# Optimization experiments

Hardware: AMD Instinct MI355X
Metric: run time of the kernel (lower is better)

## Reference

```python
import jax, jax.numpy as jnp
import numpy as np

B, S, VOCAB, HID, NH, L, SPAN = 4, 512, 25, 512, 8, 12, 512
HEAD = HID // NH
FF = 4 * HID
EPS = 1e-7  # DebertaV2 layer_norm_eps


def _ln(x, g, b):
    m = x.mean(-1, keepdims=True)
    v = ((x - m) ** 2).mean(-1, keepdims=True)
    return (x - m) / jnp.sqrt(v + EPS) * g + b


def setup_inputs() -> dict:
    key = jax.random.key(0)
    ks = iter(jax.random.split(key, 16))
    w = lambda shape: jax.random.normal(next(ks), shape, jnp.float32) * 0.05
    return {
        "x": jax.random.randint(next(ks), (B, S), 0, VOCAB),
        "attention_mask": jnp.ones((B, S), jnp.int32),
        "word_emb": w((VOCAB, HID)),
        "emb_ln_g": jnp.ones((HID,), jnp.float32),
        "emb_ln_b": jnp.zeros((HID,), jnp.float32),
        "rel_emb": w((2 * SPAN, HID)),
        "Wq": w((L, HID, HID)), "bq": jnp.zeros((L, HID), jnp.float32),
        "Wk": w((L, HID, HID)), "bk": jnp.zeros((L, HID), jnp.float32),
        "Wv": w((L, HID, HID)), "bv": jnp.zeros((L, HID), jnp.float32),
        "Wpk": w((L, HID, HID)), "bpk": jnp.zeros((L, HID), jnp.float32),
        "Wpq": w((L, HID, HID)), "bpq": jnp.zeros((L, HID), jnp.float32),
        "Wo": w((L, HID, HID)), "bo": jnp.zeros((L, HID), jnp.float32),
        "ln1_g": jnp.ones((L, HID), jnp.float32), "ln1_b": jnp.zeros((L, HID), jnp.float32),
        "W1": w((L, HID, FF)), "b1": jnp.zeros((L, FF), jnp.float32),
        "W2": w((L, FF, HID)), "b2": jnp.zeros((L, HID), jnp.float32),
        "ln2_g": jnp.ones((L, HID), jnp.float32), "ln2_b": jnp.zeros((L, HID), jnp.float32),
        "cls_w": w((VOCAB, HID)), "cls_b": jnp.zeros((VOCAB,), jnp.float32),
    }


def _forward(x, attention_mask, word_emb, emb_ln_g, emb_ln_b, rel_emb,
             Wq, bq, Wk, bk, Wv, bv, Wpk, bpk, Wpq, bpq, Wo, bo,
             ln1_g, ln1_b, W1, b1, W2, b2, ln2_g, ln2_b, cls_w, cls_b):
    mask = attention_mask.astype(jnp.float32)
    # embeddings: word only (position_biased_input=False), LN, then masked
    h = _ln(word_emb[x], emb_ln_g, emb_ln_b) * mask[..., None]

    rel = jnp.arange(S)[:, None] - jnp.arange(S)[None, :]          # q_pos - k_pos
    c2p_idx = jnp.clip(rel + SPAN, 0, 2 * SPAN - 1)[None, None]    # [1,1,S,S]
    p2c_idx = jnp.clip(-rel + SPAN, 0, 2 * SPAN - 1)[None, None]
    attm = (mask[:, None, None, :] * mask[:, None, :, None]) > 0   # [B,1,S,S]
    scale = jnp.sqrt(jnp.float32(HEAD * 3))                        # scale_factor = 1 + len(pos_att_type)
    neg = jnp.finfo(jnp.float32).min

    def heads(t):  # [B,S,HID] -> [B,NH,S,HEAD]
        return t.reshape(B, S, NH, HEAD).transpose(0, 2, 1, 3)

    for l in range(L):
        q = heads(h @ Wq[l] + bq[l])
        k = heads(h @ Wk[l] + bk[l])
        v = heads(h @ Wv[l] + bv[l])
        # projected relative-position embeddings: [NH, 2*SPAN, HEAD]
        pk = (rel_emb @ Wpk[l] + bpk[l]).reshape(2 * SPAN, NH, HEAD).transpose(1, 0, 2)
        pq = (rel_emb @ Wpq[l] + bpq[l]).reshape(2 * SPAN, NH, HEAD).transpose(1, 0, 2)

        scores = jnp.einsum('bhqd,bhkd->bhqk', q, k)
        # c2p: query content vs key position, gathered at clamp(rel+span)
        c2p = jnp.take_along_axis(jnp.einsum('bhqd,hpd->bhqp', q, pk), c2p_idx, axis=-1)
        # p2c: key content vs query position, gathered at clamp(-rel+span) then transposed
        p2c = jnp.take_along_axis(jnp.einsum('bhkd,hpd->bhkp', k, pq), p2c_idx, axis=-1)
        scores = (scores + c2p + jnp.swapaxes(p2c, -1, -2)) / scale

        scores = jnp.where(attm, scores, neg)
        probs = jnp.where(attm, jax.nn.softmax(scores, axis=-1), 0.0)  # XSoftmax
        ctx = jnp.einsum('bhqk,bhkd->bhqd', probs, v).transpose(0, 2, 1, 3).reshape(B, S, HID)
        h = _ln(ctx @ Wo[l] + bo[l] + h, ln1_g[l], ln1_b[l])
        f = jax.nn.gelu(h @ W1[l] + b1[l], approximate=False) @ W2[l] + b2[l]
        h = _ln(f + h, ln2_g[l], ln2_b[l])

    logits = h @ cls_w.T + cls_b
    return h, logits


def reference(x, attention_mask, word_emb, emb_ln_g, emb_ln_b, rel_emb,
              Wq, bq, Wk, bk, Wv, bv, Wpk, bpk, Wpq, bpq, Wo, bo,
              ln1_g, ln1_b, W1, b1, W2, b2, ln2_g, ln2_b, cls_w, cls_b):
    return _forward(x, attention_mask, word_emb, emb_ln_g, emb_ln_b, rel_emb,
                    Wq, bq, Wk, bk, Wv, bv, Wpk, bpk, Wpq, bpq, Wo, bo,
                    ln1_g, ln1_b, W1, b1, W2, b2, ln2_g, ln2_b, cls_w, cls_b)
```

## Files before the change

kernel.cpp:

```cpp
#include <hip/hip_runtime.h>
#include <hip/hip_bf16.h>

#define BATCH  4
#define SEQ    512
#define TOK    (BATCH*SEQ)
#define HID    512
#define NHEAD  8
#define HEAD   64
#define FFDIM  2048
#define NLAYER 12
#define SPAN2  1024
#define VOCAB  25
#define LNEPS  1e-7f
#define NEG_BIG -3.0e38f

typedef __attribute__((ext_vector_type(8))) short bf16x8;
typedef __attribute__((ext_vector_type(4))) float floatx4;

#define MFMA16(a, b, c) __builtin_amdgcn_mfma_f32_16x16x32_bf16((a), (b), (c), 0, 0, 0)

__device__ __forceinline__ float b2f(unsigned short u) {
    return __uint_as_float(((unsigned int)u) << 16);
}
__device__ __forceinline__ unsigned short f2b(float f) {
    __hip_bfloat16 h = __float2bfloat16(f);
    return *(unsigned short*)&h;
}

__device__ __forceinline__ float wave_sum(float v) {
    #pragma unroll
    for (int o = 1; o < 64; o <<= 1) v += __shfl_xor(v, o);
    return v;
}

__device__ __forceinline__ void ln_finish(const float (&v)[8], const float* __restrict__ g,
                                          const float* __restrict__ bb, int lane, float maskf,
                                          size_t base, float* __restrict__ h,
                                          unsigned short* __restrict__ hb) {
    float sum = 0.f;
    #pragma unroll
    for (int j = 0; j < 8; j++) sum += v[j];
    float mean = wave_sum(sum) * (1.0f / HID);
    float d[8]; float var = 0.f;
    #pragma unroll
    for (int j = 0; j < 8; j++) { d[j] = v[j] - mean; var += d[j] * d[j]; }
    float rstd = rsqrtf(wave_sum(var) * (1.0f / HID) + LNEPS);
    const float* gp = g + lane * 8; const float* bp = bb + lane * 8;
    float4 g0 = *(const float4*)gp, g1 = *(const float4*)(gp + 4);
    float4 b0 = *(const float4*)bp, b1 = *(const float4*)(bp + 4);
    float gg[8] = {g0.x, g0.y, g0.z, g0.w, g1.x, g1.y, g1.z, g1.w};
    float bv[8] = {b0.x, b0.y, b0.z, b0.w, b1.x, b1.y, b1.z, b1.w};
    float o8[8];
    #pragma unroll
    for (int j = 0; j < 8; j++) o8[j] = (d[j] * rstd * gg[j] + bv[j]) * maskf;
    *(float4*)(h + base)     = make_float4(o8[0], o8[1], o8[2], o8[3]);
    *(float4*)(h + base + 4) = make_float4(o8[4], o8[5], o8[6], o8[7]);
    uint4 pb;
    pb.x = (unsigned int)f2b(o8[0]) | ((unsigned int)f2b(o8[1]) << 16);
    pb.y = (unsigned int)f2b(o8[2]) | ((unsigned int)f2b(o8[3]) << 16);
    pb.z = (unsigned int)f2b(o8[4]) | ((unsigned int)f2b(o8[5]) << 16);
    pb.w = (unsigned int)f2b(o8[6]) | ((unsigned int)f2b(o8[7]) << 16);
    *(uint4*)(hb + base) = pb;
}

__global__ void embed_ln_kernel(const int* __restrict__ x, const int* __restrict__ am,
                                const float* __restrict__ word_emb,
                                const float* __restrict__ g, const float* __restrict__ bb,
                                float* __restrict__ h, unsigned short* __restrict__ hb) {
    int wv = threadIdx.x >> 6, lane = threadIdx.x & 63;
    int t = blockIdx.x * 4 + wv;
    const float* we = word_emb + (size_t)x[t] * HID + lane * 8;
    float4 va = *(const float4*)we, vb2 = *(const float4*)(we + 4);
    float v[8] = {va.x, va.y, va.z, va.w, vb2.x, vb2.y, vb2.z, vb2.w};
    ln_finish(v, g, bb, lane, (float)am[t], (size_t)t * HID + lane * 8, h, hb);
}

__global__ void add_ln_kernel(const float* __restrict__ tmp,
                              const float* __restrict__ g, const float* __restrict__ bb,
                              float* __restrict__ h, unsigned short* __restrict__ hb) {
    int wv = threadIdx.x >> 6, lane = threadIdx.x & 63;
    int t = blockIdx.x * 4 + wv;
    size_t base = (size_t)t * HID + lane * 8;
    float4 ta = *(const float4*)(tmp + base), tb = *(const float4*)(tmp + base + 4);
    float4 ha = *(const float4*)(h + base),  hbb = *(const float4*)(h + base + 4);
    float v[8] = {ta.x + ha.x, ta.y + ha.y, ta.z + ha.z, ta.w + ha.w,
                  tb.x + hbb.x, tb.y + hbb.y, tb.z + hbb.z, tb.w + hbb.w};
    ln_finish(v, g, bb, lane, 1.0f, base, h, hb);
}

__global__ void add_ln2_kernel(const float* __restrict__ t1a, const float* __restrict__ t1b,
                               const float* __restrict__ g, const float* __restrict__ bb,
                               float* __restrict__ h, unsigned short* __restrict__ hb) {
    int wv = threadIdx.x >> 6, lane = threadIdx.x & 63;
    int t = blockIdx.x * 4 + wv;
    size_t base = (size_t)t * HID + lane * 8;
    float4 aa = *(const float4*)(t1a + base), ab = *(const float4*)(t1a + base + 4);
    float4 ba = *(const float4*)(t1b + base), bbv = *(const float4*)(t1b + base + 4);
    float4 ha = *(const float4*)(h + base),  hb2 = *(const float4*)(h + base + 4);
    float v[8] = {aa.x + ba.x + ha.x, aa.y + ba.y + ha.y, aa.z + ba.z + ha.z, aa.w + ba.w + ha.w,
                  ab.x + bbv.x + hb2.x, ab.y + bbv.y + hb2.y, ab.z + bbv.z + hb2.z, ab.w + bbv.w + hb2.w};
    ln_finish(v, g, bb, lane, 1.0f, base, h, hb);
}

__global__ void cvt_rel_kernel(const float* __restrict__ in, unsigned short* __restrict__ out) {
    int i = (blockIdx.x * 256 + threadIdx.x) * 4;
    float4 v = *(const float4*)(in + i);
    out[i] = f2b(v.x); out[i+1] = f2b(v.y); out[i+2] = f2b(v.z); out[i+3] = f2b(v.w);
}

__global__ void tcvt_kernel(const float* __restrict__ in, unsigned short* __restrict__ out,
                            int K, int N) {
    __shared__ float tile[32][33];
    int l = blockIdx.z;
    const float* ip = in + (size_t)l * K * N;
    unsigned short* op = out + (size_t)l * K * N;
    int kb = blockIdx.y * 32, nb = blockIdx.x * 32;
    int tx = threadIdx.x, ty = threadIdx.y;
    #pragma unroll
    for (int i = 0; i < 32; i += 8) tile[ty + i][tx] = ip[(size_t)(kb + ty + i) * N + nb + tx];
    __syncthreads();
    #pragma unroll
    for (int i = 0; i < 32; i += 8) op[(size_t)(nb + ty + i) * K + kb + tx] = f2b(tile[tx][ty + i]);
}

__global__ void tcvt6_kernel(const float* __restrict__ Wq, const float* __restrict__ Wk,
                             const float* __restrict__ Wv, const float* __restrict__ Wpk,
                             const float* __restrict__ Wpq, const float* __restrict__ Wo,
                             unsigned short* __restrict__ out) {
    __shared__ float tile[32][33];
    int z = blockIdx.z, l = z / 6, w = z - l * 6;
    const float* src = w == 0 ? Wq : w == 1 ? Wk : w == 2 ? Wv : w == 3 ? Wpk : w == 4 ? Wpq : Wo;
    const float* ip = src + (size_t)l * HID * HID;
    unsigned short* op = out + ((size_t)w * NLAYER + l) * HID * HID;
    int kb = blockIdx.y * 32, nb = blockIdx.x * 32;
    int tx = threadIdx.x, ty = threadIdx.y;
    #pragma unroll
    for (int i = 0; i < 32; i += 8) tile[ty + i][tx] = ip[(size_t)(kb + ty + i) * HID + nb + tx];
    __syncthreads();
    #pragma unroll
    for (int i = 0; i < 32; i += 8) op[(size_t)(nb + ty + i) * HID + kb + tx] = f2b(tile[tx][ty + i]);
}

__device__ __forceinline__ void gemm_core128(
    const unsigned short* __restrict__ A, const unsigned short* __restrict__ Bt,
    int row0, int col0, int K, int kbeg, int kend,
    floatx4 (&acc)[4][2], unsigned short (&As)[2][128][72], unsigned short (&Bs)[2][64][72]) {
    int tid = threadIdx.x;
    int lane = tid & 63, wid = tid >> 6;
    int wm = wid >> 1, wn = wid & 1;
    int m16 = lane & 15, quad = lane >> 4;
    int asr = tid >> 1, asc = (tid & 1) * 32;
    int bsr = tid >> 2, bsc = (tid & 3) * 16;
    const unsigned short* Ag = A + (size_t)(row0 + asr) * K + asc;
    const unsigned short* Bg = Bt + (size_t)(col0 + bsr) * K + bsc;

    uint4 a0 = *(const uint4*)(Ag + kbeg),      a1 = *(const uint4*)(Ag + kbeg + 8);
    uint4 a2 = *(const uint4*)(Ag + kbeg + 16), a3 = *(const uint4*)(Ag + kbeg + 24);
    uint4 b0 = *(const uint4*)(Bg + kbeg),      b1 = *(const uint4*)(Bg + kbeg + 8);
    *(uint4*)&As[0][asr][asc]      = a0;
    *(uint4*)&As[0][asr][asc + 8]  = a1;
    *(uint4*)&As[0][asr][asc + 16] = a2;
    *(uint4*)&As[0][asr][asc + 24] = a3;
    *(uint4*)&Bs[0][bsr][bsc]      = b0;
    *(uint4*)&Bs[0][bsr][bsc + 8]  = b1;
    __syncthreads();

    int cur = 0;
    for (int k0 = kbeg; k0 < kend; k0 += 64) {
        int k1 = k0 + 64;
        bool more = k1 < kend;
        if (more) {
            a0 = *(const uint4*)(Ag + k1);      a1 = *(const uint4*)(Ag + k1 + 8);
            a2 = *(const uint4*)(Ag + k1 + 16); a3 = *(const uint4*)(Ag + k1 + 24);
            b0 = *(const uint4*)(Bg + k1);      b1 = *(const uint4*)(Bg + k1 + 8);
        }
        #pragma unroll
        for (int kk = 0; kk < 2; kk++) {
            bf16x8 bf0 = *(const bf16x8*)&Bs[cur][wn * 32 + m16][kk * 32 + quad * 8];
            bf16x8 bf1 = *(const bf16x8*)&Bs[cur][wn * 32 + 16 + m16][kk * 32 + quad * 8];
            #pragma unroll
            for (int mi = 0; mi < 4; mi++) {
                bf16x8 af = *(const bf16x8*)&As[cur][wm * 64 + mi * 16 + m16][kk * 32 + quad * 8];
                acc[mi][0] = MFMA16(af, bf0, acc[mi][0]);
                acc[mi][1] = MFMA16(af, bf1, acc[mi][1]);
            }
        }
        if (more) {
            *(uint4*)&As[cur ^ 1][asr][asc]      = a0;
            *(uint4*)&As[cur ^ 1][asr][asc + 8]  = a1;
            *(uint4*)&As[cur ^ 1][asr][asc + 16] = a2;
            *(uint4*)&As[cur ^ 1][asr][asc + 24] = a3;
            *(uint4*)&Bs[cur ^ 1][bsr][bsc]      = b0;
            *(uint4*)&Bs[cur ^ 1][bsr][bsc + 8]  = b1;
            __syncthreads();
            cur ^= 1;
        }
    }
}

template<bool OUT_BF16, bool GELU, int SPLITK>
__global__ __launch_bounds__(256, 2) void gemm_bt2(
    const unsigned short* __restrict__ A, const unsigned short* __restrict__ Bt,
    const float* __restrict__ bias, void* __restrict__ Cp, int N, int K) {
    __shared__ unsigned short As[2][128][72], Bs[2][64][72];
    int row0 = blockIdx.y * 128, col0 = blockIdx.x * 64;
    int kseg = K / SPLITK;
    int kbeg = kseg * blockIdx.z, kend = kbeg + kseg;
    floatx4 acc[4][2];
    #pragma unroll
    for (int mi = 0; mi < 4; mi++)
        #pragma unroll
        for (int ni = 0; ni < 2; ni++) acc[mi][ni] = (floatx4){0.f, 0.f, 0.f, 0.f};
    gemm_core128(A, Bt, row0, col0, K, kbeg, kend, acc, As, Bs);

    int tid = threadIdx.x, lane = tid & 63, wid = tid >> 6;
    int wm = wid >> 1, wn = wid & 1, m16 = lane & 15, quad = lane >> 4;
    size_t outoff = (size_t)blockIdx.z * (size_t)(gridDim.y << 7) * N;
    #pragma unroll
    for (int ni = 0; ni < 2; ni++) {
        int colg = col0 + wn * 32 + ni * 16 + m16;
        float bval = (SPLITK == 1 || blockIdx.z == 0) ? bias[colg] : 0.0f;
        #pragma unroll
        for (int mi = 0; mi < 4; mi++) {
            #pragma unroll
            for (int r = 0; r < 4; r++) {
                int rowg = row0 + wm * 64 + mi * 16 + quad * 4 + r;
                float v = acc[mi][ni][r] + bval;
                if (GELU) v = 0.5f * v * (1.0f + erff(v * 0.70710678118654752f));
                if (OUT_BF16) ((unsigned short*)Cp)[(size_t)rowg * N + colg] = f2b(v);
                else          ((float*)Cp)[outoff + (size_t)rowg * N + colg] = v;
            }
        }
    }
}

__global__ __launch_bounds__(256, 2) void qkvp_gemm(
    const unsigned short* __restrict__ hb, const unsigned short* __restrict__ relb,
    const unsigned short* __restrict__ Wqt, const unsigned short* __restrict__ Wkt,
    const unsigned short* __restrict__ Wvt, const unsigned short* __restrict__ Wpkt,
    const unsigned short* __restrict__ Wpqt,
    const float* __restrict__ bq, const float* __restrict__ bk, const float* __restrict__ bv,
    const float* __restrict__ bpk, const float* __restrict__ bpq,
    unsigned short* __restrict__ qb, unsigned short* __restrict__ kb,
    unsigned short* __restrict__ vb, unsigned short* __restrict__ pkb,
    unsigned short* __restrict__ pqb) {
    __shared__ unsigned short As[2][128][72], Bs[2][64][72];
    int bid = blockIdx.x;
    int xcd = bid & 7, slot = bid >> 3;
    int op, j;
    if (xcd < 6) { op = xcd >> 1; j = slot * 2 + (xcd & 1); }
    else         { op = xcd - 3;  j = slot; }
    int trow = j >> 3, tcol = j & 7;
    const unsigned short* A; const unsigned short* Bt; const float* bias; unsigned short* C;
    if (op < 3) {
        A = hb;
        Bt   = op == 0 ? Wqt : op == 1 ? Wkt : Wvt;
        bias = op == 0 ? bq  : op == 1 ? bk  : bv;
        C    = op == 0 ? qb  : op == 1 ? kb  : vb;
    } else {
        A = relb;
        Bt   = op == 3 ? Wpkt : Wpqt;
        bias = op == 3 ? bpk  : bpq;
        C    = op == 3 ? pkb  : pqb;
    }
    floatx4 acc[4][2];
    #pragma unroll
    for (int mi = 0; mi < 4; mi++)
        #pragma unroll
        for (int ni = 0; ni < 2; ni++) acc[mi][ni] = (floatx4){0.f, 0.f, 0.f, 0.f};
    gemm_core128(A, Bt, trow * 128, tcol * 64, HID, 0, HID, acc, As, Bs);

    int tid = threadIdx.x, lane = tid & 63, wid = tid >> 6;
    int wm = wid >> 1, wn = wid & 1, m16 = lane & 15, quad = lane >> 4;
    #pragma unroll
    for (int ni = 0; ni < 2; ni++) {
        int colg = tcol * 64 + wn * 32 + ni * 16 + m16;
        float bval = bias[colg];
        #pragma unroll
        for (int mi = 0; mi < 4; mi++) {
            #pragma unroll
            for (int r = 0; r < 4; r++) {
                int rowg = trow * 128 + wm * 64 + mi * 16 + quad * 4 + r;
                C[(size_t)rowg * HID + colg] = f2b(acc[mi][ni][r] + bval);
            }
        }
    }
}

template<bool OUT_BF16, bool GELU>
__global__ __launch_bounds__(256) void mfma_gemm(
    const unsigned short* __restrict__ A, const float* __restrict__ B,
    const float* __restrict__ bias, void* __restrict__ Cp, int N, int K) {
    __shared__ unsigned short As[64][72];
    __shared__ unsigned short Bs[64][72];
    int tid = threadIdx.x;
    int lane = tid & 63, wid = tid >> 6;
    int wm = wid >> 1, wn = wid & 1;
    int row0 = blockIdx.y * 64, col0 = blockIdx.x * 64;
    int m16 = lane & 15, quad = lane >> 4;

    int ar = tid >> 2, ac = (tid & 3) << 4;
    int bk = (tid >> 3) << 1, bn = (tid & 7) << 3;

    const unsigned short* Ag = A + (size_t)(row0 + ar) * K + ac;
    const float* Bg = B + (size_t)bk * N + col0 + bn;

    floatx4 acc[2][2];
    #pragma unroll
    for (int mi = 0; mi < 2; mi++)
        #pragma unroll
        for (int ni = 0; ni < 2; ni++) acc[mi][ni] = (floatx4){0.f, 0.f, 0.f, 0.f};

    for (int k0 = 0; k0 < K; k0 += 64) {
        uint4 av0 = *(const uint4*)(Ag + k0);
        uint4 av1 = *(const uint4*)(Ag + k0 + 8);
        const float* br0 = Bg + (size_t)k0 * N;
        const float* br1 = br0 + N;
        float4 b00 = *(const float4*)br0, b01 = *(const float4*)(br0 + 4);
        float4 b10 = *(const float4*)br1, b11 = *(const float4*)(br1 + 4);
        *(uint4*)&As[ar][ac] = av0;
        *(uint4*)&As[ar][ac + 8] = av1;
        float lo[8] = {b00.x, b00.y, b00.z, b00.w, b01.x, b01.y, b01.z, b01.w};
        float hi[8] = {b10.x, b10.y, b10.z, b10.w, b11.x, b11.y, b11.z, b11.w};
        #pragma unroll
        for (int i = 0; i < 8; i++) {
            unsigned int p = (unsigned int)f2b(lo[i]) | ((unsigned int)f2b(hi[i]) << 16);
            *(unsigned int*)&Bs[bn + i][bk] = p;
        }
        __syncthreads();
        #pragma unroll
        for (int kk = 0; kk < 2; kk++) {
            bf16x8 a0 = *(const bf16x8*)&As[wm * 32 + m16][kk * 32 + quad * 8];
            bf16x8 a1 = *(const bf16x8*)&As[wm * 32 + 16 + m16][kk * 32 + quad * 8];
            bf16x8 b0 = *(const bf16x8*)&Bs[wn * 32 + m16][kk * 32 + quad * 8];
            bf16x8 b1 = *(const bf16x8*)&Bs[wn * 32 + 16 + m16][kk * 32 + quad * 8];
            acc[0][0] = MFMA16(a0, b0, acc[0][0]);
            acc[0][1] = MFMA16(a0, b1, acc[0][1]);
            acc[1][0] = MFMA16(a1, b0, acc[1][0]);
            acc[1][1] = MFMA16(a1, b1, acc[1][1]);
        }
        __syncthreads();
    }
    #pragma unroll
    for (int ni = 0; ni < 2; ni++) {
        int colg = col0 + wn * 32 + ni * 16 + m16;
        float bv = bias[colg];
        #pragma unroll
        for (int mi = 0; mi < 2; mi++) {
            #pragma unroll
            for (int r = 0; r < 4; r++) {
                int rowg = row0 + wm * 32 + mi * 16 + quad * 4 + r;
                float v = acc[mi][ni][r] + bv;
                if (GELU) v = 0.5f * v * (1.0f + erff(v * 0.70710678118654752f));
                if (OUT_BF16) ((unsigned short*)Cp)[(size_t)rowg * N + colg] = f2b(v);
                else          ((float*)Cp)[(size_t)rowg * N + colg] = v;
            }
        }
    }
}

__global__ __launch_bounds__(256, 2) void attn_kernel(
    const unsigned short* __restrict__ Q, const unsigned short* __restrict__ K,
    const unsigned short* __restrict__ V,
    const unsigned short* __restrict__ PK, const unsigned short* __restrict__ PQ,
    const int* __restrict__ am, unsigned short* __restrict__ ctx) {
    __shared__ unsigned short Ks[2][32][72];
    __shared__ unsigned short Vt[2][64][40];
    __shared__ float Afs[4][16][49];
    __shared__ float Bfs[4][32][50];
    __shared__ unsigned short Pls[4][16][40];
    __shared__ int mkk[2][32];
    __shared__ float mergeML[2][2][16];

    int bid = blockIdx.x;
    int hh = bid & 7;
    int b  = (bid >> 3) & 3;
    int q0 = (bid >> 5) * 32;
    int tid = threadIdx.x;
    int lane = tid & 63, wave = tid >> 6;
    int u = wave >> 1;
    int s = wave & 1;
    int quad = lane >> 4, m16 = lane & 15;
    const float inv_scale = 0.07216878364870323f;

    const unsigned short* qg = Q + (size_t)(b * SEQ + q0 + u * 16 + m16) * HID + hh * HEAD;
    bf16x8 qf0 = *(const bf16x8*)(qg + quad * 8);
    bf16x8 qf1 = *(const bf16x8*)(qg + 32 + quad * 8);

    int sr = tid >> 3;
    int sc = (tid & 7) * 8;
    int vkey = ((sc >> 3) & 3) << 3;

    floatx4 accO[4];
    #pragma unroll
    for (int nt = 0; nt < 4; nt++) accO[nt] = (floatx4){0.f, 0.f, 0.f, 0.f};
    float mreg[4] = {NEG_BIG, NEG_BIG, NEG_BIG, NEG_BIG};
    float lreg[4] = {0.f, 0.f, 0.f, 0.f};

    auto loadPQ = [&](int t, bf16x8 (&pkf)[3][2], bf16x8 (&pqf)[3][2]) {
        int P0  = q0 - 32 * t + 481;
        int P20 = 32 * t - q0 + 481;
        int Jb  = 16 - 16 * u;
        #pragma unroll
        for (int nt = 0; nt < 3; nt++) {
            int prow = P0 + 16 * u + nt * 16 + m16;
            const unsigned short* pg = PK + (size_t)prow * HID + hh * HEAD + quad * 8;
            pkf[nt][0] = *(const bf16x8*)pg;
            pkf[nt][1] = *(const bf16x8*)(pg + 32);
            int prow2 = P20 + Jb + nt * 16 + m16;
            if (prow2 > 1023) prow2 = 1023;
            const unsigned short* pg2 = PQ + (size_t)prow2 * HID + hh * HEAD + quad * 8;
            pqf[nt][0] = *(const bf16x8*)pg2;
            pqf[nt][1] = *(const bf16x8*)(pg2 + 32);
        }
    };

    auto stageKV = [&](int ph) {
        #pragma unroll
        for (int sl = 0; sl < 2; sl++) {
            int k0 = ph * 64 + sl * 32;
            const unsigned short* kg = K + (size_t)(b * SEQ + k0 + sr) * HID + hh * HEAD + sc;
            *(uint4*)&Ks[sl][sr][sc] = *(const uint4*)kg;
            uint4 vv = *(const uint4*)(V + (size_t)(b * SEQ + k0 + sr) * HID + hh * HEAD + sc);
            unsigned short* vp = (unsigned short*)&vv;
            #pragma unroll
            for (int j = 0; j < 8; j++) Vt[sl][sc + j][sr ^ vkey] = vp[j];
        }
        if (tid < 64) mkk[tid >> 5][tid & 31] = am[b * SEQ + ph * 64 + tid];
    };

    auto computePhase = [&](bf16x8 (&pkf)[3][2], bf16x8 (&pqf)[3][2]) {
        floatx4 accS[2];
        accS[0] = (floatx4){0.f, 0.f, 0.f, 0.f};
        accS[1] = (floatx4){0.f, 0.f, 0.f, 0.f};
        #pragma unroll
        for (int n = 0; n < 2; n++) {
            bf16x8 kfa = *(const bf16x8*)&Ks[s][n * 16 + m16][quad * 8];
            bf16x8 kfb = *(const bf16x8*)&Ks[s][n * 16 + m16][32 + quad * 8];
            accS[n] = MFMA16(qf0, kfa, accS[n]);
            accS[n] = MFMA16(qf1, kfb, accS[n]);
        }
        {
            floatx4 accA[3];
            #pragma unroll
            for (int nt = 0; nt < 3; nt++) {
                accA[nt] = (floatx4){0.f, 0.f, 0.f, 0.f};
                accA[nt] = MFMA16(qf0, pkf[nt][0], accA[nt]);
                accA[nt] = MFMA16(qf1, pkf[nt][1], accA[nt]);
            }
            #pragma unroll
            for (int nt = 0; nt < 3; nt++)
                #pragma unroll
                for (int r = 0; r < 4; r++)
                    Afs[wave][quad * 4 + r][nt * 16 + m16] = accA[nt][r];
        }
        {
            floatx4 accB[2][3];
            #pragma unroll
            for (int mt = 0; mt < 2; mt++) {
                bf16x8 afa = *(const bf16x8*)&Ks[s][mt * 16 + m16][quad * 8];
                bf16x8 afb = *(const bf16x8*)&Ks[s][mt * 16 + m16][32 + quad * 8];
                #pragma unroll
                for (int nt = 0; nt < 3; nt++) {
                    accB[mt][nt] = (floatx4){0.f, 0.f, 0.f, 0.f};
                    accB[mt][nt] = MFMA16(afa, pqf[nt][0], accB[mt][nt]);
                    accB[mt][nt] = MFMA16(afb, pqf[nt][1], accB[mt][nt]);
                }
            }
            #pragma unroll
            for (int mt = 0; mt < 2; mt++)
                #pragma unroll
                for (int nt = 0; nt < 3; nt++)
                    #pragma unroll
                    for (int r = 0; r < 4; r++)
                        Bfs[wave][mt * 16 + quad * 4 + r][nt * 16 + m16] = accB[mt][nt][r];
        }
        float sv[2][4];
        float tmax[4] = {NEG_BIG, NEG_BIG, NEG_BIG, NEG_BIG};
        #pragma unroll
        for (int n = 0; n < 2; n++) {
            #pragma unroll
            for (int r = 0; r < 4; r++) {
                int qq = quad * 4 + r;
                int kc = n * 16 + m16;
                float av = Afs[wave][qq][qq - kc + 31];
                float bv = Bfs[wave][kc][kc - qq + 15];
                float x = (accS[n][r] + av + bv) * inv_scale;
                x = mkk[s][kc] ? x : NEG_BIG;
                sv[n][r] = x;
                tmax[r] = fmaxf(tmax[r], x);
            }
        }
        float alpha[4], psum[4];
        #pragma unroll
        for (int r = 0; r < 4; r++) {
            float tm = tmax[r];
            tm = fmaxf(tm, __shfl_xor(tm, 1));
            tm = fmaxf(tm, __shfl_xor(tm, 2));
            tm = fmaxf(tm, __shfl_xor(tm, 4));
            tm = fmaxf(tm, __shfl_xor(tm, 8));
            float mo = mreg[r];
            float mn = fmaxf(mo, tm);
            alpha[r] = __expf(mo - mn);
            mreg[r] = mn;
        }
        #pragma unroll
        for (int r = 0; r < 4; r++) psum[r] = 0.f;
        #pragma unroll
        for (int n = 0; n < 2; n++) {
            #pragma unroll
            for (int r = 0; r < 4; r++) {
                float p = (sv[n][r] > -1.5e38f) ? __expf(sv[n][r] - mreg[r]) : 0.0f;
                unsigned short pb = f2b(p);
                Pls[wave][quad * 4 + r][n * 16 + m16] = pb;
                psum[r] += b2f(pb);
            }
        }
        #pragma unroll
        for (int r = 0; r < 4; r++) {
            float ps = psum[r];
            ps += __shfl_xor(ps, 1);
            ps += __shfl_xor(ps, 2);
            ps += __shfl_xor(ps, 4);
            ps += __shfl_xor(ps, 8);
            lreg[r] = lreg[r] * alpha[r] + ps;
        }
        #pragma unroll
        for (int nt = 0; nt < 4; nt++)
            #pragma unroll
            for (int r = 0; r < 4; r++) accO[nt][r] *= alpha[r];
        {
            bf16x8 pf = *(const bf16x8*)&Pls[wave][m16][quad * 8];
            #pragma unroll
            for (int nt = 0; nt < 4; nt++) {
                int d = nt * 16 + m16;
                int kq = (quad ^ ((d >> 3) & 3)) * 8;
                bf16x8 vf = *(const bf16x8*)&Vt[s][d][kq];
                accO[nt] = MFMA16(pf, vf, accO[nt]);
            }
        }
    };

    bf16x8 pkfA[3][2], pqfA[3][2], pkfB[3][2], pqfB[3][2];
    loadPQ(s, pkfA, pqfA);
    #pragma unroll
    for (int pp = 0; pp < 4; pp++) {
        {
            int ph = 2 * pp;
            __syncthreads();
            stageKV(ph);
            __syncthreads();
            if (ph < 7) loadPQ(2 * (ph + 1) + s, pkfB, pqfB);
            computePhase(pkfA, pqfA);
        }
        {
            int ph = 2 * pp + 1;
            __syncthreads();
            stageKV(ph);
            __syncthreads();
            if (ph < 7) loadPQ(2 * (ph + 1) + s, pkfA, pqfA);
            computePhase(pkfB, pqfB);
        }
    }

    __syncthreads();
    float* mo = &Bfs[0][0][0];
    if (s == 1) {
        #pragma unroll
        for (int nt = 0; nt < 4; nt++)
            #pragma unroll
            for (int r = 0; r < 4; r++)
                mo[u * 1056 + (quad * 4 + r) * 66 + nt * 16 + m16] = accO[nt][r];
        if (m16 == 0) {
            #pragma unroll
            for (int r = 0; r < 4; r++) {
                mergeML[u][0][quad * 4 + r] = mreg[r];
                mergeML[u][1][quad * 4 + r] = lreg[r];
            }
        }
    }
    __syncthreads();
    if (s == 0) {
        #pragma unroll
        for (int r = 0; r < 4; r++) {
            int row = quad * 4 + r;
            float m1 = mergeML[u][0][row], l1 = mergeML[u][1][row];
            float m0 = mreg[r], l0 = lreg[r];
            float mt = fmaxf(m0, m1);
            float a0 = __expf(m0 - mt), a1 = __expf(m1 - mt);
            float lt = l0 * a0 + l1 * a1;
            float inv = lt > 0.0f ? 1.0f / lt : 0.0f;
            inv *= (float)am[b * SEQ + q0 + u * 16 + row];
            #pragma unroll
            for (int nt = 0; nt < 4; nt++) {
                float o1 = mo[u * 1056 + row * 66 + nt * 16 + m16];
                float val = (accO[nt][r] * a0 + o1 * a1) * inv;
                ctx[(size_t)(b * SEQ + q0 + u * 16 + row) * HID + hh * HEAD + nt * 16 + m16] = f2b(val);
            }
        }
    }
}

__global__ void copy_f_kernel(const float* __restrict__ in, float* __restrict__ out, int n) {
    int i = blockIdx.x * 256 + threadIdx.x;
    if (i < n) out[i] = in[i];
}
__global__ void cls_kernel(const float* __restrict__ h, const float* __restrict__ cls_w,
                           const float* __restrict__ cls_b, float* __restrict__ out) {
    int t = blockIdx.x, v = threadIdx.x;
    if (v < VOCAB) {
        const float* hr = h + (size_t)t * HID;
        const float* wr = cls_w + (size_t)v * HID;
        float acc = cls_b[v];
        for (int d = 0; d < HID; d++) acc += hr[d] * wr[d];
        out[t * VOCAB + v] = acc;
    }
}

extern "C" void kernel_launch(void* const* d_in, const int* in_sizes, int n_in,
                              void* d_out, int out_size, void* d_ws, size_t ws_size,
                              hipStream_t stream) {
    const int* x     = (const int*)d_in[0];
    const int* am    = (const int*)d_in[1];
    const float* word_emb = (const float*)d_in[2];
    const float* emb_g    = (const float*)d_in[3];
    const float* emb_b    = (const float*)d_in[4];
    const float* rel_emb  = (const float*)d_in[5];
    const float* Wq  = (const float*)d_in[6];  const float* bq  = (const float*)d_in[7];
    const float* Wk  = (const float*)d_in[8];  const float* bk  = (const float*)d_in[9];
    const float* Wv  = (const float*)d_in[10]; const float* bv  = (const float*)d_in[11];
    const float* Wpk = (const float*)d_in[12]; const float* bpk = (const float*)d_in[13];
    const float* Wpq = (const float*)d_in[14]; const float* bpq = (const float*)d_in[15];
    const float* Wo  = (const float*)d_in[16]; const float* bo  = (const float*)d_in[17];
    const float* ln1g = (const float*)d_in[18]; const float* ln1b = (const float*)d_in[19];
    const float* W1  = (const float*)d_in[20]; const float* b1  = (const float*)d_in[21];
    const float* W2  = (const float*)d_in[22]; const float* b2  = (const float*)d_in[23];
    const float* ln2g = (const float*)d_in[24]; const float* ln2b = (const float*)d_in[25];
    const float* cls_w = (const float*)d_in[26]; const float* cls_b = (const float*)d_in[27];

    char* wsb = (char*)d_ws;
    const size_t NEED_BIG = 107u << 20;

    if (ws_size >= NEED_BIG) {
        float* h  = (float*)wsb;
        float* t1 = (float*)(wsb + (4u << 20));
        float* t2 = (float*)(wsb + (8u << 20));
        unsigned short* qb   = (unsigned short*)(wsb + (12u << 20));
        unsigned short* kb   = (unsigned short*)(wsb + (14u << 20));
        unsigned short* vb   = (unsigned short*)(wsb + (16u << 20));
        unsigned short* pkb  = (unsigned short*)(wsb + (18u << 20));
        unsigned short* pqb  = (unsigned short*)(wsb + (19u << 20));
        unsigned short* relb = (unsigned short*)(wsb + (20u << 20));
        unsigned short* hb   = (unsigned short*)(wsb + (21u << 20));
        unsigned short* ctx  = hb;
        unsigned short* ffb  = qb;
        unsigned short* Wqt  = (unsigned short*)(wsb + (23u << 20));
        unsigned short* W1t  = (unsigned short*)(wsb + (59u << 20));
        unsigned short* W2t  = (unsigned short*)(wsb + (83u << 20));

        const size_t M512 = (size_t)HID * HID;

        tcvt6_kernel<<<dim3(16, 16, 72), dim3(32, 8), 0, stream>>>(Wq, Wk, Wv, Wpk, Wpq, Wo, Wqt);
        tcvt_kernel<<<dim3(64, 16, 12), dim3(32, 8), 0, stream>>>(W1, W1t, HID, FFDIM);
        tcvt_kernel<<<dim3(16, 64, 12), dim3(32, 8), 0, stream>>>(W2, W2t, FFDIM, HID);
        cvt_rel_kernel<<<dim3(SPAN2 * HID / 1024), dim3(256), 0, stream>>>(rel_emb, relb);
        embed_ln_kernel<<<dim3(TOK / 4), dim3(256), 0, stream>>>(x, am, word_emb, emb_g, emb_b, h, hb);

        for (int l = 0; l < NLAYER; l++) {
            qkvp_gemm<<<dim3(512), dim3(256), 0, stream>>>(
                hb, relb,
                Wqt + (size_t)(0 * NLAYER + l) * M512, Wqt + (size_t)(1 * NLAYER + l) * M512,
                Wqt + (size_t)(2 * NLAYER + l) * M512, Wqt + (size_t)(3 * NLAYER + l) * M512,
                Wqt + (size_t)(4 * NLAYER + l) * M512,
                bq + l * HID, bk + l * HID, bv + l * HID, bpk + l * HID, bpq + l * HID,
                qb, kb, vb, pkb, pqb);

            attn_kernel<<<dim3(512), dim3(256), 0, stream>>>(
                qb, kb, vb, pkb, pqb, am, ctx);

            gemm_bt2<false, false, 2><<<dim3(HID / 64, TOK / 128, 2), dim3(256), 0, stream>>>(
                ctx, Wqt + (size_t)(5 * NLAYER + l) * M512, bo + l * HID, t1, HID, HID);
            add_ln2_kernel<<<dim3(TOK / 4), dim3(256), 0, stream>>>(t1, t2, ln1g + l * HID, ln1b + l * HID, h, hb);

            gemm_bt2<true, true, 1><<<dim3(FFDIM / 64, TOK / 128, 1), dim3(256), 0, stream>>>(
                hb, W1t + (size_t)l * HID * FFDIM, b1 + l * FFDIM, ffb, FFDIM, HID);
            gemm_bt2<false, false, 2><<<dim3(HID / 64, TOK / 128, 2), dim3(256), 0, stream>>>(
                ffb, W2t + (size_t)l * HID * FFDIM, b2 + l * HID, t1, HID, FFDIM);
            add_ln2_kernel<<<dim3(TOK / 4), dim3(256), 0, stream>>>(t1, t2, ln2g + l * HID, ln2b + l * HID, h, hb);
        }

        float* out_f = (float*)d_out;
        copy_f_kernel<<<dim3(TOK * HID / 256), dim3(256), 0, stream>>>(h, out_f, TOK * HID);
        cls_kernel<<<dim3(TOK), dim3(32), 0, stream>>>(h, cls_w, cls_b, out_f + TOK * HID);
        return;
    }

    const size_t NEEDED = 19u << 20;
    if (ws_size < NEEDED) return;
    float* h  = (float*)wsb;
    float* t1 = (float*)(wsb + (4u << 20));
    unsigned short* qb   = (unsigned short*)(wsb + (8u << 20));
    unsigned short* kb   = qb  + (1u << 20);
    unsigned short* vb   = kb  + (1u << 20);
    unsigned short* pkb  = vb  + (1u << 20);
    unsigned short* pqb  = pkb + (1u << 19);
    unsigned short* relb = (unsigned short*)(wsb + (16u << 20));
    unsigned short* hb   = (unsigned short*)(wsb + (17u << 20));
    unsigned short* ctx  = hb;
    unsigned short* ffb  = qb;

    cvt_rel_kernel<<<dim3(SPAN2 * HID / 1024), dim3(256), 0, stream>>>(rel_emb, relb);
    embed_ln_kernel<<<dim3(TOK / 4), dim3(256), 0, stream>>>(x, am, word_emb, emb_g, emb_b, h, hb);

    for (int l = 0; l < NLAYER; l++) {
        const float* Wq_l = Wq + (size_t)l * HID * HID;
        const float* Wk_l = Wk + (size_t)l * HID * HID;
        const float* Wv_l = Wv + (size_t)l * HID * HID;
        const float* Wo_l = Wo + (size_t)l * HID * HID;
        const float* Wpk_l = Wpk + (size_t)l * HID * HID;
        const float* Wpq_l = Wpq + (size_t)l * HID * HID;
        const float* W1_l = W1 + (size_t)l * HID * FFDIM;
        const float* W2_l = W2 + (size_t)l * FFDIM * HID;

        mfma_gemm<true,  false><<<dim3(HID/64, TOK/64),   dim3(256), 0, stream>>>(hb,   Wq_l,  bq + l*HID,  qb,  HID, HID);
        mfma_gemm<true,  false><<<dim3(HID/64, TOK/64),   dim3(256), 0, stream>>>(hb,   Wk_l,  bk + l*HID,  kb,  HID, HID);
        mfma_gemm<true,  false><<<dim3(HID/64, TOK/64),   dim3(256), 0, stream>>>(hb,   Wv_l,  bv + l*HID,  vb,  HID, HID);
        mfma_gemm<true,  false><<<dim3(HID/64, SPAN2/64), dim3(256), 0, stream>>>(relb, Wpk_l, bpk + l*HID, pkb, HID, HID);
        mfma_gemm<true,  false><<<dim3(HID/64, SPAN2/64), dim3(256), 0, stream>>>(relb, Wpq_l, bpq + l*HID, pqb, HID, HID);

        attn_kernel<<<dim3(512), dim3(256), 0, stream>>>(qb, kb, vb, pkb, pqb, am, ctx);

        mfma_gemm<false, false><<<dim3(HID/64, TOK/64),   dim3(256), 0, stream>>>(ctx,  Wo_l,  bo + l*HID,  t1,  HID, HID);
        add_ln_kernel<<<dim3(TOK / 4), dim3(256), 0, stream>>>(t1, ln1g + l*HID, ln1b + l*HID, h, hb);

        mfma_gemm<true,  true ><<<dim3(FFDIM/64, TOK/64), dim3(256), 0, stream>>>(hb,   W1_l,  b1 + l*FFDIM, ffb, FFDIM, HID);
        mfma_gemm<false, false><<<dim3(HID/64, TOK/64),   dim3(256), 0, stream>>>(ffb,  W2_l,  b2 + l*HID,  t1,  HID, FFDIM);
        add_ln_kernel<<<dim3(TOK / 4), dim3(256), 0, stream>>>(t1, ln2g + l*HID, ln2b + l*HID, h, hb);
    }

    float* out_f = (float*)d_out;
    copy_f_kernel<<<dim3(TOK*HID/256), dim3(256), 0, stream>>>(h, out_f, TOK*HID);
    cls_kernel<<<dim3(TOK), dim3(32), 0, stream>>>(h, cls_w, cls_b, out_f + TOK*HID);
}
```

Measured before the change: 1.424 ms.

## Use direct global-to-LDS loads with XOR-swizzled tiles in GEMM core

Replaces the register-staged global loads and LDS stores in the shared GEMM core with global_load_lds instructions that write tiles straight into LDS. Tiles lose their padding and use an XOR swizzle on the 16-byte column chunk to avoid bank conflicts, and the next tile is issued before computing on the current one. This is meant to cut VGPR pressure and the extra LDS write instructions in every projection and FFN GEMM. It relies on the barrier at the end of each iteration to cover the async loads.

```diff
diff --git a/kernel.cpp b/kernel.cpp
--- a/kernel.cpp
+++ b/kernel.cpp
@@ -27,6 +27,11 @@
     return *(unsigned short*)&h;
 }
 
+__device__ __forceinline__ void gload16(const unsigned short* g, unsigned short* lds_base) {
+    __builtin_amdgcn_global_load_lds((const __attribute__((address_space(1))) void*)g,
+                                     (__attribute__((address_space(3))) void*)lds_base, 16, 0, 0);
+}
+
 __device__ __forceinline__ float wave_sum(float v) {
     #pragma unroll
     for (int o = 1; o < 64; o <<= 1) v += __shfl_xor(v, o);
@@ -144,57 +149,61 @@
 __device__ __forceinline__ void gemm_core128(
     const unsigned short* __restrict__ A, const unsigned short* __restrict__ Bt,
     int row0, int col0, int K, int kbeg, int kend,
-    floatx4 (&acc)[4][2], unsigned short (&As)[2][128][72], unsigned short (&Bs)[2][64][72]) {
+    floatx4 (&acc)[4][2], unsigned short* AsB, unsigned short* BsB) {
     int tid = threadIdx.x;
-    int lane = tid & 63, wid = tid >> 6;
-    int wm = wid >> 1, wn = wid & 1;
+    int lane = tid & 63, w = tid >> 6;
+    int wm = w >> 1, wn = w & 1;
     int m16 = lane & 15, quad = lane >> 4;
-    int asr = tid >> 1, asc = (tid & 1) * 32;
-    int bsr = tid >> 2, bsc = (tid & 3) * 16;
-    const unsigned short* Ag = A + (size_t)(row0 + asr) * K + asc;
-    const unsigned short* Bg = Bt + (size_t)(col0 + bsr) * K + bsc;
-
-    uint4 a0 = *(const uint4*)(Ag + kbeg),      a1 = *(const uint4*)(Ag + kbeg + 8);
-    uint4 a2 = *(const uint4*)(Ag + kbeg + 16), a3 = *(const uint4*)(Ag + kbeg + 24);
-    uint4 b0 = *(const uint4*)(Bg + kbeg),      b1 = *(const uint4*)(Bg + kbeg + 8);
-    *(uint4*)&As[0][asr][asc]      = a0;
-    *(uint4*)&As[0][asr][asc + 8]  = a1;
-    *(uint4*)&As[0][asr][asc + 16] = a2;
-    *(uint4*)&As[0][asr][asc + 24] = a3;
-    *(uint4*)&Bs[0][bsr][bsc]      = b0;
-    *(uint4*)&Bs[0][bsr][bsc + 8]  = b1;
+
+    int arow[4], acol[4], brow[2], bcol[2];
+    #pragma unroll
+    for (int c = 0; c < 4; c++) {
+        int o = ((w * 4 + c) * 64 + lane) * 16;
+        int r = o >> 7;
+        arow[c] = r;
+        acol[c] = (o & 127) ^ ((r & 7) << 4);
+    }
+    #pragma unroll
+    for (int c = 0; c < 2; c++) {
+        int o = ((w * 2 + c) * 64 + lane) * 16;
+        int r = o >> 7;
+        brow[c] = r;
+        bcol[c] = (o & 127) ^ ((r & 7) << 4);
+    }
+
+    auto stage = [&](int bf, int k0) {
+        #pragma unroll
+        for (int c = 0; c < 4; c++)
+            gload16(A + (size_t)(row0 + arow[c]) * K + k0 + (acol[c] >> 1),
+                    AsB + bf * 8192 + (w * 4 + c) * 512);
+        #pragma unroll
+        for (int c = 0; c < 2; c++)
+            gload16(Bt + (size_t)(col0 + brow[c]) * K + k0 + (bcol[c] >> 1),
+                    BsB + bf * 4096 + (w * 2 + c) * 512);
+    };
+
+    stage(0, kbeg);
     __syncthreads();
-
     int cur = 0;
     for (int k0 = kbeg; k0 < kend; k0 += 64) {
-        int k1 = k0 + 64;
-        bool more = k1 < kend;
-        if (more) {
-            a0 = *(const uint4*)(Ag + k1);      a1 = *(const uint4*)(Ag + k1 + 8);
-            a2 = *(const uint4*)(Ag + k1 + 16); a3 = *(const uint4*)(Ag + k1 + 24);
-            b0 = *(const uint4*)(Bg + k1);      b1 = *(const uint4*)(Bg + k1 + 8);
-        }
+        if (k0 + 64 < kend) stage(cur ^ 1, k0 + 64);
+        const char* Ab = (const char*)(AsB + cur * 8192);
+        const char* Bb = (const char*)(BsB + cur * 4096);
+        int br0 = wn * 32 + m16, br1 = wn * 32 + 16 + m16;
         #pragma unroll
         for (int kk = 0; kk < 2; kk++) {
-            bf16x8 bf0 = *(const bf16x8*)&Bs[cur][wn * 32 + m16][kk * 32 + quad * 8];
-            bf16x8 bf1 = *(const bf16x8*)&Bs[cur][wn * 32 + 16 + m16][kk * 32 + quad * 8];
+            bf16x8 bf0 = *(const bf16x8*)(Bb + ((((br0 << 7) + kk * 64 + quad * 16)) ^ ((m16 & 7) << 4)));
+            bf16x8 bf1 = *(const bf16x8*)(Bb + ((((br1 << 7) + kk * 64 + quad * 16)) ^ ((m16 & 7) << 4)));
             #pragma unroll
             for (int mi = 0; mi < 4; mi++) {
-                bf16x8 af = *(const bf16x8*)&As[cur][wm * 64 + mi * 16 + m16][kk * 32 + quad * 8];
+                int ar = wm * 64 + mi * 16 + m16;
+                bf16x8 af = *(const bf16x8*)(Ab + ((((ar << 7) + kk * 64 + quad * 16)) ^ ((m16 & 7) << 4)));
                 acc[mi][0] = MFMA16(af, bf0, acc[mi][0]);
                 acc[mi][1] = MFMA16(af, bf1, acc[mi][1]);
             }
         }
-        if (more) {
-            *(uint4*)&As[cur ^ 1][asr][asc]      = a0;
-            *(uint4*)&As[cur ^ 1][asr][asc + 8]  = a1;
-            *(uint4*)&As[cur ^ 1][asr][asc + 16] = a2;
-            *(uint4*)&As[cur ^ 1][asr][asc + 24] = a3;
-            *(uint4*)&Bs[cur ^ 1][bsr][bsc]      = b0;
-            *(uint4*)&Bs[cur ^ 1][bsr][bsc + 8]  = b1;
-            __syncthreads();
-            cur ^= 1;
-        }
+        __syncthreads();
+        cur ^= 1;
     }
 }
 
@@ -202,7 +211,7 @@
 __global__ __launch_bounds__(256, 2) void gemm_bt2(
     const unsigned short* __restrict__ A, const unsigned short* __restrict__ Bt,
     const float* __restrict__ bias, void* __restrict__ Cp, int N, int K) {
-    __shared__ unsigned short As[2][128][72], Bs[2][64][72];
+    __shared__ unsigned short As[2][8192], Bs[2][4096];
     int row0 = blockIdx.y * 128, col0 = blockIdx.x * 64;
     int kseg = K / SPLITK;
     int kbeg = kseg * blockIdx.z, kend = kbeg + kseg;
@@ -211,7 +220,7 @@
     for (int mi = 0; mi < 4; mi++)
         #pragma unroll
         for (int ni = 0; ni < 2; ni++) acc[mi][ni] = (floatx4){0.f, 0.f, 0.f, 0.f};
-    gemm_core128(A, Bt, row0, col0, K, kbeg, kend, acc, As, Bs);
+    gemm_core128(A, Bt, row0, col0, K, kbeg, kend, acc, &As[0][0], &Bs[0][0]);
 
     int tid = threadIdx.x, lane = tid & 63, wid = tid >> 6;
     int wm = wid >> 1, wn = wid & 1, m16 = lane & 15, quad = lane >> 4;
@@ -244,7 +253,7 @@
     unsigned short* __restrict__ qb, unsigned short* __restrict__ kb,
     unsigned short* __restrict__ vb, unsigned short* __restrict__ pkb,
     unsigned short* __restrict__ pqb) {
-    __shared__ unsigned short As[2][128][72], Bs[2][64][72];
+    __shared__ unsigned short As[2][8192], Bs[2][4096];
     int bid = blockIdx.x;
     int xcd = bid & 7, slot = bid >> 3;
     int op, j;
@@ -268,7 +277,7 @@
     for (int mi = 0; mi < 4; mi++)
         #pragma unroll
         for (int ni = 0; ni < 2; ni++) acc[mi][ni] = (floatx4){0.f, 0.f, 0.f, 0.f};
-    gemm_core128(A, Bt, trow * 128, tcol * 64, HID, 0, HID, acc, As, Bs);
+    gemm_core128(A, Bt, trow * 128, tcol * 64, HID, 0, HID, acc, &As[0][0], &Bs[0][0]);
 
     int tid = threadIdx.x, lane = tid & 63, wid = tid >> 6;
     int wm = wid >> 1, wn = wid & 1, m16 = lane & 15, quad = lane >> 4;
```

Result: no change. 1.424 ms (-0.0%).
